# Performance work log

Hardware: AMD Instinct MI355X
Metric: run time of the kernel (lower is better)

Reference implementation:

```python
import jax, jax.numpy as jnp
import numpy as np

B, NQ, NK, D, DV = 16, 2048, 2048, 128, 128


def setup_inputs() -> dict:
    key = jax.random.key(0)
    kq, kk, kv, kl = jax.random.split(key, 4)
    return {
        "queries": jax.random.normal(kq, (B, NQ, D), dtype=jnp.float32),
        "keys": jax.random.normal(kk, (B, NK, D), dtype=jnp.float32),
        "values": jax.random.normal(kv, (B, NK, DV), dtype=jnp.float32),
        "valid_lens": jax.random.randint(kl, (B,), 1, NK + 1, dtype=jnp.int32),
    }


def reference(queries, keys, values, valid_lens):
    d = queries.shape[-1]
    # scores: [B, NQ, NK]
    scores = jnp.einsum("bqd,bkd->bqk", queries, keys) / jnp.sqrt(jnp.float32(d))
    # mask positions >= valid_len with -1e6 (matches sequence_mask semantics)
    key_pos = jnp.arange(scores.shape[-1], dtype=jnp.int32)  # [NK]
    mask = key_pos[None, None, :] < valid_lens[:, None, None]  # [B,1,NK] -> broadcast over queries
    scores = jnp.where(mask, scores, jnp.float32(-1000000.0))
    attn = jax.nn.softmax(scores, axis=-1)
    # dropout p=0.0 -> identity
    return jnp.einsum("bqk,bkv->bqv", attn, values)
```

## Files before the change

### kernel.cpp

```cpp
#include <hip/hip_runtime.h>


#define B_   16
#define NQ_  2048
#define NK_  2048
#define D_   128
#define DV_  128
#define NTASK_ 512

typedef unsigned short ushort;
typedef __attribute__((ext_vector_type(4))) float          f32x4;
typedef __attribute__((ext_vector_type(8))) __bf16         bf16x8;
typedef __attribute__((ext_vector_type(8))) unsigned short ushort8v;
typedef __attribute__((ext_vector_type(4))) unsigned int   uint4v;

#ifdef __has_builtin
#if __has_builtin(__builtin_amdgcn_cvt_pk_bf16_f32)
#define HAVE_CVT_PK_BF16 1
#endif
#endif

__device__ __forceinline__ ushort f2bf(float f) {
    unsigned u = __builtin_bit_cast(unsigned, f);
    return (ushort)((u + 0x8000u) >> 16);
}
__device__ __forceinline__ unsigned f2bf2(float a, float b) {
#ifdef HAVE_CVT_PK_BF16
    auto t = __builtin_amdgcn_cvt_pk_bf16_f32(a, b);
    return __builtin_bit_cast(unsigned, t);
#else
    return (unsigned)f2bf(a) | ((unsigned)f2bf(b) << 16);
#endif
}
__device__ __forceinline__ float bfpair_sum(unsigned u) {
    float lo = __builtin_bit_cast(float, u << 16);
    float hi = __builtin_bit_cast(float, u & 0xffff0000u);
    return lo + hi;
}
__device__ __forceinline__ void gl_lds16(const ushort* g, ushort* l) {
    __builtin_amdgcn_global_load_lds(
        (const __attribute__((address_space(1))) void*)g,
        (__attribute__((address_space(3))) void*)l, 16, 0, 0);
}

__global__ __launch_bounds__(256) void convert_kv(
    const float* __restrict__ K, const float* __restrict__ V,
    const int* __restrict__ vlen, ushort* __restrict__ Kb, ushort* __restrict__ Vtb)
{
    const int id = blockIdx.x;
    const int b  = id & 15, kt = id >> 4;
    if (kt >= ((vlen[b] + 63) >> 6)) return;
    const int tid = threadIdx.x;
    const float* gK = K + ((size_t)b * NK_ + kt * 64) * D_;
    const float* gV = V + ((size_t)b * NK_ + kt * 64) * DV_;
    ushort* tK = Kb  + ((size_t)b * 32 + kt) * 8192;
    ushort* tV = Vtb + ((size_t)b * 32 + kt) * 8192;

    #pragma unroll
    for (int i = 0; i < 4; ++i) {
        int u = i * 256 + tid;
        int key = u >> 4, d8 = u & 15;
        const float* p = gK + key * D_ + d8 * 8;
        f32x4 a0 = *(const f32x4*)p;
        f32x4 a1 = *(const f32x4*)(p + 4);
        uint4v w;
        w[0] = f2bf2(a0[0], a0[1]); w[1] = f2bf2(a0[2], a0[3]);
        w[2] = f2bf2(a1[0], a1[1]); w[3] = f2bf2(a1[2], a1[3]);
        *(uint4v*)&tK[key * 128 + ((d8 ^ (key & 7)) << 3)] = w;
    }
    #pragma unroll
    for (int i = 0; i < 4; ++i) {
        int u = i * 256 + tid;
        int dv = u & 127, kg = u >> 7;
        const float* vp = gV + (size_t)(kg * 8) * DV_ + dv;
        float v[8];
        #pragma unroll
        for (int j = 0; j < 8; ++j) v[j] = vp[(size_t)j * DV_];
        uint4v w;
        w[0] = f2bf2(v[0], v[1]); w[1] = f2bf2(v[2], v[3]);
        w[2] = f2bf2(v[4], v[5]); w[3] = f2bf2(v[6], v[7]);
        *(uint4v*)&tV[dv * 64 + ((kg ^ (dv & 7)) << 3)] = w;
    }
}

__global__ __launch_bounds__(512, 4) void attn_fwd(
    const float* __restrict__ Q, const int* __restrict__ vlen,
    const ushort* __restrict__ Kb, const ushort* __restrict__ Vtb,
    float* __restrict__ Out)
{
    __shared__ ushort KVbuf[2][16384];
    __shared__ float  lsh[2][64];
    __shared__ int    ssch[16];
    float* Osh = (float*)&KVbuf[0][0];

    const int tid  = threadIdx.x;
    const int w    = tid >> 6;
    const int wq   = w >> 1;
    const int wk   = w & 1;
    const int L    = tid & 63;
    const int col  = L & 15;
    const int quad = L >> 4;

    if (tid < 16) {
        int my = vlen[tid];
        int rank = 0;
        for (int o = 0; o < 16; ++o) {
            int vo = vlen[o];
            if (vo > my || (vo == my && o < tid)) ++rank;
        }
        ssch[rank] = tid;
    }
    __syncthreads();

    const int e     = blockIdx.x;
    const int p_    = (e & 255) >> 5;
    const int b     = (e >> 8) ? ssch[15 - p_] : ssch[p_];
    const int qbase = (e & 31) * 64;
    const int vl    = vlen[b];
    const int ntiles = (vl + 63) >> 6;

    const float qscale = 0.12751743f;
    bf16x8 qf[4];
    {
        const int qrow = qbase + wq * 16 + col;
        const float* gQ = Q + ((size_t)b * NQ_ + qrow) * D_;
        #pragma unroll
        for (int c = 0; c < 4; ++c) {
            const float* pp = gQ + c * 32 + quad * 8;
            f32x4 a0 = *(const f32x4*)pp;
            f32x4 a1 = *(const f32x4*)(pp + 4);
            uint4v us;
            us[0] = f2bf2(a0[0] * qscale, a0[1] * qscale);
            us[1] = f2bf2(a0[2] * qscale, a0[3] * qscale);
            us[2] = f2bf2(a1[0] * qscale, a1[1] * qscale);
            us[3] = f2bf2(a1[2] * qscale, a1[3] * qscale);
            qf[c] = __builtin_bit_cast(bf16x8, us);
        }
    }

    f32x4 o[8];
    #pragma unroll
    for (int d = 0; d < 8; ++d) o[d] = (f32x4){0.f, 0.f, 0.f, 0.f};
    float l_run = 0.f;

    const ushort* tKb = Kb  + (size_t)b * 32 * 8192;
    const ushort* tVb = Vtb + (size_t)b * 32 * 8192;

    #define ISSUE_DMA(KT, BUF)                                               \
        do {                                                                 \
            const ushort* gk = tKb + (size_t)(KT) * 8192;                    \
            const ushort* gv = tVb + (size_t)(KT) * 8192;                    \
            _Pragma("unroll")                                                \
            for (int i = 0; i < 2; ++i) {                                    \
                int off = (i * 512 + tid) * 8;                               \
                gl_lds16(gk + off, &KVbuf[BUF][off]);                        \
                gl_lds16(gv + off, &KVbuf[BUF][8192 + off]);                 \
            }                                                                \
        } while (0)

    ISSUE_DMA(0, 0);

    const int swz = col & 7;

    for (int kt = 0; kt < ntiles; ++kt) {
        const int buf = kt & 1;
        __syncthreads();
        if (kt + 1 < ntiles) ISSUE_DMA(kt + 1, buf ^ 1);

        const ushort* Kt = &KVbuf[buf][0];
        const ushort* Vt = &KVbuf[buf][8192];

        f32x4 s0 = (f32x4){0.f,0.f,0.f,0.f};
        f32x4 s1 = (f32x4){0.f,0.f,0.f,0.f};
        __builtin_amdgcn_s_setprio(1);
        {
            const int key0 = (wk * 32 + col) * 128;
            #pragma unroll
            for (int c = 0; c < 4; ++c) {
                bf16x8 kb = __builtin_bit_cast(bf16x8, *(const ushort8v*)
                    &Kt[key0 + (((c * 4 + quad) ^ swz) << 3)]);
                s0 = __builtin_amdgcn_mfma_f32_16x16x32_bf16(kb, qf[c], s0, 0, 0, 0);
            }
            #pragma unroll
            for (int c = 0; c < 4; ++c) {
                bf16x8 kb = __builtin_bit_cast(bf16x8, *(const ushort8v*)
                    &Kt[key0 + 16 * 128 + (((c * 4 + quad) ^ swz) << 3)]);
                s1 = __builtin_amdgcn_mfma_f32_16x16x32_bf16(kb, qf[c], s1, 0, 0, 0);
            }
        }
        __builtin_amdgcn_s_setprio(0);

        const int rem = vl - kt * 64 - wk * 32;
        if (rem < 32) {
            #pragma unroll
            for (int rr = 0; rr < 4; ++rr) {
                if (quad * 4 + rr >= rem)      s0[rr] = -1e30f;
                if (16 + quad * 4 + rr >= rem) s1[rr] = -1e30f;
            }
        }

        unsigned wA = f2bf2(exp2f(s0[0]), exp2f(s0[1]));
        unsigned wB = f2bf2(exp2f(s0[2]), exp2f(s0[3]));
        unsigned wC = f2bf2(exp2f(s1[0]), exp2f(s1[1]));
        unsigned wD = f2bf2(exp2f(s1[2]), exp2f(s1[3]));
        l_run += bfpair_sum(wA) + bfpair_sum(wB) + bfpair_sum(wC) + bfpair_sum(wD);

        asm("v_permlane32_swap_b32 %0, %1" : "+v"(wA), "+v"(wC));
        asm("v_permlane32_swap_b32 %0, %1" : "+v"(wB), "+v"(wD));
        asm("v_permlane16_swap_b32 %0, %1" : "+v"(wA), "+v"(wC));
        asm("v_permlane16_swap_b32 %0, %1" : "+v"(wB), "+v"(wD));
        uint4v pw;
        pw[0] = wA; pw[1] = wB; pw[2] = wC; pw[3] = wD;
        bf16x8 pa = __builtin_bit_cast(bf16x8, pw);

        __builtin_amdgcn_s_setprio(1);
        #pragma unroll
        for (int dvc = 0; dvc < 8; ++dvc) {
            const int dv = dvc * 16 + col;
            bf16x8 vb = __builtin_bit_cast(bf16x8, *(const ushort8v*)
                &Vt[dv * 64 + (((wk * 4 + quad) ^ swz) << 3)]);
            o[dvc] = __builtin_amdgcn_mfma_f32_16x16x32_bf16(pa, vb, o[dvc], 0, 0, 0);
        }
        __builtin_amdgcn_s_setprio(0);
    }
    #undef ISSUE_DMA

    l_run += __shfl_xor(l_run, 16, 64);
    l_run += __shfl_xor(l_run, 32, 64);

    __syncthreads();

    if (L < 16) lsh[wk][wq * 16 + L] = l_run;
    #pragma unroll
    for (int dvc = 0; dvc < 8; ++dvc)
        #pragma unroll
        for (int rr = 0; rr < 4; ++rr)
            Osh[wk * 8192 + (wq * 16 + quad * 4 + rr) * 128 + dvc * 16 + col]
                = o[dvc][rr];
    __syncthreads();

    float* gO = Out + ((size_t)b * NQ_ + qbase) * DV_;
    #pragma unroll
    for (int i = 0; i < 4; ++i) {
        int idx = i * 512 + tid;
        int row = idx >> 5;
        int dq  = idx & 31;
        f32x4 a0 = *(const f32x4*)&Osh[row * 128 + dq * 4];
        f32x4 a1 = *(const f32x4*)&Osh[8192 + row * 128 + dq * 4];
        float linv = 1.0f / (lsh[0][row] + lsh[1][row]);
        *(f32x4*)&gO[(size_t)row * DV_ + dq * 4] = (a0 + a1) * linv;
    }
}

extern "C" void kernel_launch(void* const* d_in, const int* in_sizes, int n_in,
                              void* d_out, int out_size, void* d_ws, size_t ws_size,
                              hipStream_t stream) {
    const float* Q  = (const float*)d_in[0];
    const float* K  = (const float*)d_in[1];
    const float* V  = (const float*)d_in[2];
    const int*   vl = (const int*)d_in[3];
    float* out = (float*)d_out;

    char* ws = (char*)d_ws;
    ushort* Kbuf = (ushort*)(ws + 4096);
    ushort* Vbuf = Kbuf + (size_t)B_ * 32 * 8192;

    convert_kv<<<dim3(512, 1, 1), dim3(256, 1, 1), 0, stream>>>(K, V, vl, Kbuf, Vbuf);
    attn_fwd<<<dim3(NTASK_, 1, 1), dim3(512, 1, 1), 0, stream>>>(
        Q, vl, Kbuf, Vbuf, out);
}
```

Measured before the change: 132.2 us.

## Process two 16-row query groups per wave with 256-thread blocks

Halves the block to 4 waves while keeping 64 query rows per block, so each wave now computes two 16-row query groups. Each K and V fragment read from LDS feeds two MFMAs, cutting LDS traffic per FLOP. The block-to-batch/query mapping is reordered so consecutive blocks cover different batches. The cost is roughly doubled accumulator registers and fewer waves available to hide latency.

```diff
diff --git a/kernel.cpp b/kernel.cpp
--- a/kernel.cpp
+++ b/kernel.cpp
@@ -83,7 +83,7 @@
     }
 }
 
-__global__ __launch_bounds__(512, 4) void attn_fwd(
+__global__ __launch_bounds__(256, 2) void attn_fwd(
     const float* __restrict__ Q, const int* __restrict__ vlen,
     const ushort* __restrict__ Kb, const ushort* __restrict__ Vtb,
     float* __restrict__ Out)
@@ -113,16 +113,17 @@
     __syncthreads();
 
     const int e     = blockIdx.x;
-    const int p_    = (e & 255) >> 5;
-    const int b     = (e >> 8) ? ssch[15 - p_] : ssch[p_];
-    const int qbase = (e & 31) * 64;
+    const int p_    = e & 7;
+    const int b     = ((e >> 3) & 1) ? ssch[15 - p_] : ssch[p_];
+    const int qbase = (e >> 4) * 64;
     const int vl    = vlen[b];
     const int ntiles = (vl + 63) >> 6;
 
     const float qscale = 0.12751743f;
-    bf16x8 qf[4];
-    {
-        const int qrow = qbase + wq * 16 + col;
+    bf16x8 qf[2][4];
+    #pragma unroll
+    for (int q16 = 0; q16 < 2; ++q16) {
+        const int qrow = qbase + wq * 32 + q16 * 16 + col;
         const float* gQ = Q + ((size_t)b * NQ_ + qrow) * D_;
         #pragma unroll
         for (int c = 0; c < 4; ++c) {
@@ -134,14 +135,16 @@
             us[1] = f2bf2(a0[2] * qscale, a0[3] * qscale);
             us[2] = f2bf2(a1[0] * qscale, a1[1] * qscale);
             us[3] = f2bf2(a1[2] * qscale, a1[3] * qscale);
-            qf[c] = __builtin_bit_cast(bf16x8, us);
-        }
-    }
-
-    f32x4 o[8];
-    #pragma unroll
-    for (int d = 0; d < 8; ++d) o[d] = (f32x4){0.f, 0.f, 0.f, 0.f};
-    float l_run = 0.f;
+            qf[q16][c] = __builtin_bit_cast(bf16x8, us);
+        }
+    }
+
+    f32x4 o[2][8];
+    #pragma unroll
+    for (int q16 = 0; q16 < 2; ++q16)
+        #pragma unroll
+        for (int d = 0; d < 8; ++d) o[q16][d] = (f32x4){0.f, 0.f, 0.f, 0.f};
+    float l_run[2] = {0.f, 0.f};
 
     const ushort* tKb = Kb  + (size_t)b * 32 * 8192;
     const ushort* tVb = Vtb + (size_t)b * 32 * 8192;
@@ -151,8 +154,8 @@
             const ushort* gk = tKb + (size_t)(KT) * 8192;                    \
             const ushort* gv = tVb + (size_t)(KT) * 8192;                    \
             _Pragma("unroll")                                                \
-            for (int i = 0; i < 2; ++i) {                                    \
-                int off = (i * 512 + tid) * 8;                               \
+            for (int i = 0; i < 4; ++i) {                                    \
+                int off = (i * 256 + tid) * 8;                               \
                 gl_lds16(gk + off, &KVbuf[BUF][off]);                        \
                 gl_lds16(gv + off, &KVbuf[BUF][8192 + off]);                 \
             }                                                                \
@@ -170,22 +173,21 @@
         const ushort* Kt = &KVbuf[buf][0];
         const ushort* Vt = &KVbuf[buf][8192];
 
-        f32x4 s0 = (f32x4){0.f,0.f,0.f,0.f};
-        f32x4 s1 = (f32x4){0.f,0.f,0.f,0.f};
+        f32x4 s[2][2];
+        #pragma unroll
+        for (int q16 = 0; q16 < 2; ++q16)
+            #pragma unroll
+            for (int kc = 0; kc < 2; ++kc) s[q16][kc] = (f32x4){0.f,0.f,0.f,0.f};
         __builtin_amdgcn_s_setprio(1);
-        {
-            const int key0 = (wk * 32 + col) * 128;
+        #pragma unroll
+        for (int kc = 0; kc < 2; ++kc) {
+            const int kbase = (wk * 32 + kc * 16 + col) * 128;
             #pragma unroll
             for (int c = 0; c < 4; ++c) {
                 bf16x8 kb = __builtin_bit_cast(bf16x8, *(const ushort8v*)
-                    &Kt[key0 + (((c * 4 + quad) ^ swz) << 3)]);
-                s0 = __builtin_amdgcn_mfma_f32_16x16x32_bf16(kb, qf[c], s0, 0, 0, 0);
-            }
-            #pragma unroll
-            for (int c = 0; c < 4; ++c) {
-                bf16x8 kb = __builtin_bit_cast(bf16x8, *(const ushort8v*)
-                    &Kt[key0 + 16 * 128 + (((c * 4 + quad) ^ swz) << 3)]);
-                s1 = __builtin_amdgcn_mfma_f32_16x16x32_bf16(kb, qf[c], s1, 0, 0, 0);
+                    &Kt[kbase + (((c * 4 + quad) ^ swz) << 3)]);
+                s[0][kc] = __builtin_amdgcn_mfma_f32_16x16x32_bf16(kb, qf[0][c], s[0][kc], 0, 0, 0);
+                s[1][kc] = __builtin_amdgcn_mfma_f32_16x16x32_bf16(kb, qf[1][c], s[1][kc], 0, 0, 0);
             }
         }
         __builtin_amdgcn_s_setprio(0);
@@ -194,24 +196,31 @@
         if (rem < 32) {
             #pragma unroll
             for (int rr = 0; rr < 4; ++rr) {
-                if (quad * 4 + rr >= rem)      s0[rr] = -1e30f;
-                if (16 + quad * 4 + rr >= rem) s1[rr] = -1e30f;
+                if (quad * 4 + rr >= rem) {
+                    s[0][0][rr] = -1e30f; s[1][0][rr] = -1e30f;
+                }
+                if (16 + quad * 4 + rr >= rem) {
+                    s[0][1][rr] = -1e30f; s[1][1][rr] = -1e30f;
+                }
             }
         }
 
-        unsigned wA = f2bf2(exp2f(s0[0]), exp2f(s0[1]));
-        unsigned wB = f2bf2(exp2f(s0[2]), exp2f(s0[3]));
-        unsigned wC = f2bf2(exp2f(s1[0]), exp2f(s1[1]));
-        unsigned wD = f2bf2(exp2f(s1[2]), exp2f(s1[3]));
-        l_run += bfpair_sum(wA) + bfpair_sum(wB) + bfpair_sum(wC) + bfpair_sum(wD);
-
-        asm("v_permlane32_swap_b32 %0, %1" : "+v"(wA), "+v"(wC));
-        asm("v_permlane32_swap_b32 %0, %1" : "+v"(wB), "+v"(wD));
-        asm("v_permlane16_swap_b32 %0, %1" : "+v"(wA), "+v"(wC));
-        asm("v_permlane16_swap_b32 %0, %1" : "+v"(wB), "+v"(wD));
-        uint4v pw;
-        pw[0] = wA; pw[1] = wB; pw[2] = wC; pw[3] = wD;
-        bf16x8 pa = __builtin_bit_cast(bf16x8, pw);
+        bf16x8 pa[2];
+        #pragma unroll
+        for (int q16 = 0; q16 < 2; ++q16) {
+            unsigned wA = f2bf2(exp2f(s[q16][0][0]), exp2f(s[q16][0][1]));
+            unsigned wB = f2bf2(exp2f(s[q16][0][2]), exp2f(s[q16][0][3]));
+            unsigned wC = f2bf2(exp2f(s[q16][1][0]), exp2f(s[q16][1][1]));
+            unsigned wD = f2bf2(exp2f(s[q16][1][2]), exp2f(s[q16][1][3]));
+            l_run[q16] += bfpair_sum(wA) + bfpair_sum(wB) + bfpair_sum(wC) + bfpair_sum(wD);
+            asm("v_permlane32_swap_b32 %0, %1" : "+v"(wA), "+v"(wC));
+            asm("v_permlane32_swap_b32 %0, %1" : "+v"(wB), "+v"(wD));
+            asm("v_permlane16_swap_b32 %0, %1" : "+v"(wA), "+v"(wC));
+            asm("v_permlane16_swap_b32 %0, %1" : "+v"(wB), "+v"(wD));
+            uint4v pw;
+            pw[0] = wA; pw[1] = wB; pw[2] = wC; pw[3] = wD;
+            pa[q16] = __builtin_bit_cast(bf16x8, pw);
+        }
 
         __builtin_amdgcn_s_setprio(1);
         #pragma unroll
@@ -219,30 +228,39 @@
             const int dv = dvc * 16 + col;
             bf16x8 vb = __builtin_bit_cast(bf16x8, *(const ushort8v*)
                 &Vt[dv * 64 + (((wk * 4 + quad) ^ swz) << 3)]);
-            o[dvc] = __builtin_amdgcn_mfma_f32_16x16x32_bf16(pa, vb, o[dvc], 0, 0, 0);
+            o[0][dvc] = __builtin_amdgcn_mfma_f32_16x16x32_bf16(pa[0], vb, o[0][dvc], 0, 0, 0);
+            o[1][dvc] = __builtin_amdgcn_mfma_f32_16x16x32_bf16(pa[1], vb, o[1][dvc], 0, 0, 0);
         }
         __builtin_amdgcn_s_setprio(0);
     }
     #undef ISSUE_DMA
 
-    l_run += __shfl_xor(l_run, 16, 64);
-    l_run += __shfl_xor(l_run, 32, 64);
+    #pragma unroll
+    for (int q16 = 0; q16 < 2; ++q16) {
+        l_run[q16] += __shfl_xor(l_run[q16], 16, 64);
+        l_run[q16] += __shfl_xor(l_run[q16], 32, 64);
+    }
 
     __syncthreads();
 
-    if (L < 16) lsh[wk][wq * 16 + L] = l_run;
-    #pragma unroll
-    for (int dvc = 0; dvc < 8; ++dvc)
-        #pragma unroll
-        for (int rr = 0; rr < 4; ++rr)
-            Osh[wk * 8192 + (wq * 16 + quad * 4 + rr) * 128 + dvc * 16 + col]
-                = o[dvc][rr];
+    if (L < 16) {
+        lsh[wk][wq * 32 + L]      = l_run[0];
+        lsh[wk][wq * 32 + 16 + L] = l_run[1];
+    }
+    #pragma unroll
+    for (int q16 = 0; q16 < 2; ++q16)
+        #pragma unroll
+        for (int dvc = 0; dvc < 8; ++dvc)
+            #pragma unroll
+            for (int rr = 0; rr < 4; ++rr)
+                Osh[wk * 8192 + (wq * 32 + q16 * 16 + quad * 4 + rr) * 128 + dvc * 16 + col]
+                    = o[q16][dvc][rr];
     __syncthreads();
 
     float* gO = Out + ((size_t)b * NQ_ + qbase) * DV_;
     #pragma unroll
-    for (int i = 0; i < 4; ++i) {
-        int idx = i * 512 + tid;
+    for (int i = 0; i < 8; ++i) {
+        int idx = i * 256 + tid;
         int row = idx >> 5;
         int dq  = idx & 31;
         f32x4 a0 = *(const f32x4*)&Osh[row * 128 + dq * 4];
@@ -266,6 +284,6 @@
     ushort* Vbuf = Kbuf + (size_t)B_ * 32 * 8192;
 
     convert_kv<<<dim3(512, 1, 1), dim3(256, 1, 1), 0, stream>>>(K, V, vl, Kbuf, Vbuf);
-    attn_fwd<<<dim3(NTASK_, 1, 1), dim3(512, 1, 1), 0, stream>>>(
+    attn_fwd<<<dim3(NTASK_, 1, 1), dim3(256, 1, 1), 0, stream>>>(
         Q, vl, Kbuf, Vbuf, out);
 }
```

After: 139.3 us. 1.05x slower.

## Split long-sequence attention tasks across two blocks with atomic-flag combine

Applied to the files above, without the earlier changes.

Launches twice as many blocks and, for batches with more than 16 key tiles, splits the key range between two blocks of the same query tile. The first block to finish writes its unnormalized partial output to global memory and the second waits on a flag, adds its partial, and normalizes. This targets load imbalance from variable valid lengths, where long batches dominate the tail. In exchange it adds spin-waiting, extra global traffic, and flag resets in the convert kernel. It also combines without max rescaling, so it relies on the softmax needing no running-max correction.

```diff
diff --git a/kernel.cpp b/kernel.cpp
--- a/kernel.cpp
+++ b/kernel.cpp
@@ -6,7 +6,6 @@
 #define NK_  2048
 #define D_   128
 #define DV_  128
-#define NTASK_ 512
 
 typedef unsigned short ushort;
 typedef __attribute__((ext_vector_type(4))) float          f32x4;
@@ -45,12 +44,14 @@
 
 __global__ __launch_bounds__(256) void convert_kv(
     const float* __restrict__ K, const float* __restrict__ V,
-    const int* __restrict__ vlen, ushort* __restrict__ Kb, ushort* __restrict__ Vtb)
+    const int* __restrict__ vlen, ushort* __restrict__ Kb, ushort* __restrict__ Vtb,
+    int* __restrict__ flags)
 {
     const int id = blockIdx.x;
     const int b  = id & 15, kt = id >> 4;
+    const int tid = threadIdx.x;
+    if (id < 4) flags[id * 256 + tid] = 0;
     if (kt >= ((vlen[b] + 63) >> 6)) return;
-    const int tid = threadIdx.x;
     const float* gK = K + ((size_t)b * NK_ + kt * 64) * D_;
     const float* gV = V + ((size_t)b * NK_ + kt * 64) * DV_;
     ushort* tK = Kb  + ((size_t)b * 32 + kt) * 8192;
@@ -86,11 +87,13 @@
 __global__ __launch_bounds__(512, 4) void attn_fwd(
     const float* __restrict__ Q, const int* __restrict__ vlen,
     const ushort* __restrict__ Kb, const ushort* __restrict__ Vtb,
+    int* __restrict__ flags, float* __restrict__ wsl,
     float* __restrict__ Out)
 {
     __shared__ ushort KVbuf[2][16384];
     __shared__ float  lsh[2][64];
     __shared__ int    ssch[16];
+    __shared__ int    role_sh;
     float* Osh = (float*)&KVbuf[0][0];
 
     const int tid  = threadIdx.x;
@@ -112,12 +115,21 @@
     }
     __syncthreads();
 
-    const int e     = blockIdx.x;
-    const int p_    = (e & 255) >> 5;
-    const int b     = (e >> 8) ? ssch[15 - p_] : ssch[p_];
-    const int qbase = (e & 31) * 64;
-    const int vl    = vlen[b];
-    const int ntiles = (vl + 63) >> 6;
+    const int e       = blockIdx.x;
+    const int h       = e & 1;
+    const int pairIdx = e >> 1;
+    const int r       = pairIdx & 15;
+    const int qt      = pairIdx >> 4;
+    const int b       = ssch[r];
+    const int qbase   = qt * 64;
+    const int vl      = vlen[b];
+    const int ntiles  = (vl + 63) >> 6;
+    const int split   = (ntiles > 16);
+    if (!split && h) return;
+    const int hh    = (ntiles + 1) >> 1;
+    const int kt_lo = split ? (h ? hh : 0) : 0;
+    const int kt_hi = split ? (h ? ntiles : hh) : ntiles;
+    const int task  = (r << 5) | qt;
 
     const float qscale = 0.12751743f;
     bf16x8 qf[4];
@@ -158,14 +170,14 @@
             }                                                                \
         } while (0)
 
-    ISSUE_DMA(0, 0);
+    ISSUE_DMA(kt_lo, 0);
 
     const int swz = col & 7;
 
-    for (int kt = 0; kt < ntiles; ++kt) {
-        const int buf = kt & 1;
+    for (int kt = kt_lo; kt < kt_hi; ++kt) {
+        const int buf = (kt - kt_lo) & 1;
         __syncthreads();
-        if (kt + 1 < ntiles) ISSUE_DMA(kt + 1, buf ^ 1);
+        if (kt + 1 < kt_hi) ISSUE_DMA(kt + 1, buf ^ 1);
 
         const ushort* Kt = &KVbuf[buf][0];
         const ushort* Vt = &KVbuf[buf][8192];
@@ -240,15 +252,64 @@
     __syncthreads();
 
     float* gO = Out + ((size_t)b * NQ_ + qbase) * DV_;
-    #pragma unroll
-    for (int i = 0; i < 4; ++i) {
-        int idx = i * 512 + tid;
-        int row = idx >> 5;
-        int dq  = idx & 31;
-        f32x4 a0 = *(const f32x4*)&Osh[row * 128 + dq * 4];
-        f32x4 a1 = *(const f32x4*)&Osh[8192 + row * 128 + dq * 4];
-        float linv = 1.0f / (lsh[0][row] + lsh[1][row]);
-        *(f32x4*)&gO[(size_t)row * DV_ + dq * 4] = (a0 + a1) * linv;
+
+    if (!split) {
+        #pragma unroll
+        for (int i = 0; i < 4; ++i) {
+            int idx = i * 512 + tid;
+            int row = idx >> 5;
+            int dq  = idx & 31;
+            f32x4 a0 = *(const f32x4*)&Osh[row * 128 + dq * 4];
+            f32x4 a1 = *(const f32x4*)&Osh[8192 + row * 128 + dq * 4];
+            float linv = 1.0f / (lsh[0][row] + lsh[1][row]);
+            *(f32x4*)&gO[(size_t)row * DV_ + dq * 4] = (a0 + a1) * linv;
+        }
+        return;
+    }
+
+    if (tid < 64) wsl[task * 128 + h * 64 + tid] = lsh[0][tid] + lsh[1][tid];
+    __threadfence();
+    __syncthreads();
+    if (tid == 0)
+        role_sh = __hip_atomic_fetch_add(&flags[task], 1, __ATOMIC_ACQ_REL,
+                                         __HIP_MEMORY_SCOPE_AGENT);
+    __syncthreads();
+
+    if (role_sh == 0) {
+        #pragma unroll
+        for (int i = 0; i < 4; ++i) {
+            int idx = i * 512 + tid;
+            int row = idx >> 5;
+            int dq  = idx & 31;
+            f32x4 a0 = *(const f32x4*)&Osh[row * 128 + dq * 4];
+            f32x4 a1 = *(const f32x4*)&Osh[8192 + row * 128 + dq * 4];
+            *(f32x4*)&gO[(size_t)row * DV_ + dq * 4] = a0 + a1;
+        }
+        __threadfence();
+        __syncthreads();
+        if (tid == 0)
+            __hip_atomic_store(&flags[512 + task], 2, __ATOMIC_RELEASE,
+                               __HIP_MEMORY_SCOPE_AGENT);
+    } else {
+        if (tid == 0) {
+            while (__hip_atomic_load(&flags[512 + task], __ATOMIC_ACQUIRE,
+                                     __HIP_MEMORY_SCOPE_AGENT) != 2)
+                __builtin_amdgcn_s_sleep(2);
+            __threadfence();
+        }
+        __syncthreads();
+        #pragma unroll
+        for (int i = 0; i < 4; ++i) {
+            int idx = i * 512 + tid;
+            int row = idx >> 5;
+            int dq  = idx & 31;
+            f32x4 a0 = *(const f32x4*)&Osh[row * 128 + dq * 4];
+            f32x4 a1 = *(const f32x4*)&Osh[8192 + row * 128 + dq * 4];
+            f32x4 po = *(const f32x4*)&gO[(size_t)row * DV_ + dq * 4];
+            float lall = lsh[0][row] + lsh[1][row]
+                       + wsl[task * 128 + (1 - h) * 64 + row];
+            *(f32x4*)&gO[(size_t)row * DV_ + dq * 4] = (a0 + a1 + po) * (1.0f / lall);
+        }
     }
 }
 
@@ -262,10 +323,12 @@
     float* out = (float*)d_out;
 
     char* ws = (char*)d_ws;
-    ushort* Kbuf = (ushort*)(ws + 4096);
-    ushort* Vbuf = Kbuf + (size_t)B_ * 32 * 8192;
-
-    convert_kv<<<dim3(512, 1, 1), dim3(256, 1, 1), 0, stream>>>(K, V, vl, Kbuf, Vbuf);
-    attn_fwd<<<dim3(NTASK_, 1, 1), dim3(512, 1, 1), 0, stream>>>(
-        Q, vl, Kbuf, Vbuf, out);
-}
+    int*    flags = (int*)ws;
+    float*  wsl   = (float*)(ws + 4096);
+    ushort* Kbuf  = (ushort*)(ws + 512 * 1024);
+    ushort* Vbuf  = Kbuf + (size_t)B_ * 32 * 8192;
+
+    convert_kv<<<dim3(512, 1, 1), dim3(256, 1, 1), 0, stream>>>(K, V, vl, Kbuf, Vbuf, flags);
+    attn_fwd<<<dim3(1024, 1, 1), dim3(512, 1, 1), 0, stream>>>(
+        Q, vl, Kbuf, Vbuf, flags, wsl, out);
+}
```

Result: slower. 380.3 us (+187.8%).

## Transpose V through LDS in convert kernel and interleave attention block-to-batch mapping

Applied to the files above, without the earlier changes.

The V conversion now reads rows with coalesced vector loads, stages them in padded shared memory, then reads columns out of LDS to write the transposed swizzled bf16 layout. This replaces strided scalar global loads. Separately, the attention kernel's block index mapping is reordered so consecutive blocks alternate between long and short batches instead of grouping all query tiles of one batch. That should balance work across CUs in each wave of blocks, but it may reduce L2 reuse of the same batch's K/V.

```diff
diff --git a/kernel.cpp b/kernel.cpp
--- a/kernel.cpp
+++ b/kernel.cpp
@@ -43,10 +43,12 @@
         (__attribute__((address_space(3))) void*)l, 16, 0, 0);
 }
 
+#define VL_STRIDE 132
 __global__ __launch_bounds__(256) void convert_kv(
     const float* __restrict__ K, const float* __restrict__ V,
     const int* __restrict__ vlen, ushort* __restrict__ Kb, ushort* __restrict__ Vtb)
 {
+    __shared__ ushort Vl[64 * VL_STRIDE];
     const int id = blockIdx.x;
     const int b  = id & 15, kt = id >> 4;
     if (kt >= ((vlen[b] + 63) >> 6)) return;
@@ -68,18 +70,35 @@
         w[2] = f2bf2(a1[0], a1[1]); w[3] = f2bf2(a1[2], a1[3]);
         *(uint4v*)&tK[key * 128 + ((d8 ^ (key & 7)) << 3)] = w;
     }
+
     #pragma unroll
     for (int i = 0; i < 4; ++i) {
         int u = i * 256 + tid;
-        int dv = u & 127, kg = u >> 7;
-        const float* vp = gV + (size_t)(kg * 8) * DV_ + dv;
-        float v[8];
-        #pragma unroll
-        for (int j = 0; j < 8; ++j) v[j] = vp[(size_t)j * DV_];
+        int key = u >> 4, d8 = u & 15;
+        const float* p = gV + key * DV_ + d8 * 8;
+        f32x4 a0 = *(const f32x4*)p;
+        f32x4 a1 = *(const f32x4*)(p + 4);
         uint4v w;
-        w[0] = f2bf2(v[0], v[1]); w[1] = f2bf2(v[2], v[3]);
-        w[2] = f2bf2(v[4], v[5]); w[3] = f2bf2(v[6], v[7]);
-        *(uint4v*)&tV[dv * 64 + ((kg ^ (dv & 7)) << 3)] = w;
+        w[0] = f2bf2(a0[0], a0[1]); w[1] = f2bf2(a0[2], a0[3]);
+        w[2] = f2bf2(a1[0], a1[1]); w[3] = f2bf2(a1[2], a1[3]);
+        *(uint4v*)&Vl[key * VL_STRIDE + d8 * 8] = w;
+    }
+    __syncthreads();
+
+    #pragma unroll
+    for (int i = 0; i < 4; ++i) {
+        int u  = i * 256 + tid;
+        int c  = u & 7, dv = u >> 3;
+        int kg = c ^ (dv & 7);
+        ushort v[8];
+        #pragma unroll
+        for (int j = 0; j < 8; ++j) v[j] = Vl[(kg * 8 + j) * VL_STRIDE + dv];
+        uint4v w;
+        w[0] = (unsigned)v[0] | ((unsigned)v[1] << 16);
+        w[1] = (unsigned)v[2] | ((unsigned)v[3] << 16);
+        w[2] = (unsigned)v[4] | ((unsigned)v[5] << 16);
+        w[3] = (unsigned)v[6] | ((unsigned)v[7] << 16);
+        *(uint4v*)&tV[dv * 64 + c * 8] = w;
     }
 }
 
@@ -113,9 +132,9 @@
     __syncthreads();
 
     const int e     = blockIdx.x;
-    const int p_    = (e & 255) >> 5;
-    const int b     = (e >> 8) ? ssch[15 - p_] : ssch[p_];
-    const int qbase = (e & 31) * 64;
+    const int p_    = e & 7;
+    const int b     = ((e >> 3) & 1) ? ssch[15 - p_] : ssch[p_];
+    const int qbase = (e >> 4) * 64;
     const int vl    = vlen[b];
     const int ntiles = (vl + 63) >> 6;
 
```

Result: slower. 135.0 us (+2.1%).
